# Kernel tuning notes

Hardware: AMD Instinct MI355X
Metric: run time of the kernel (lower is better)

The kernel has to match this reference:

```python
import jax, jax.numpy as jnp
import numpy as np

TEMPERATURE = 0.5
NEG_FILL = -9e15


def setup_inputs() -> dict:
    key = jax.random.key(0)
    k1, k2 = jax.random.split(key)
    B, D = 4096, 256
    z1 = jax.random.normal(k1, (B, D), dtype=jnp.float32)
    z2 = jax.random.normal(k2, (B, D), dtype=jnp.float32)
    return {"z1": z1, "z2": z2}


def reference(z1, z2):
    B = z1.shape[0]
    z = jnp.concatenate([z1, z2], axis=0)  # [2B, D]
    # cosine similarity: normalize once, then GEMM (same math as broadcast cosine_similarity,
    # torch uses eps=1e-8 clamp on norms)
    norm = jnp.maximum(jnp.linalg.norm(z, axis=1, keepdims=True), 1e-8)
    zn = z / norm
    sim = (zn @ zn.T) / TEMPERATURE  # [2B, 2B]
    # mask self-similarity on the diagonal
    idx = jnp.arange(2 * B)
    sim = sim.at[idx, idx].set(NEG_FILL)
    labels = jnp.concatenate([jnp.arange(B) + B, jnp.arange(B)], axis=0)  # [2B]
    logp = jax.nn.log_softmax(sim, axis=1)
    loss = -jnp.mean(logp[idx, labels])
    return loss
```

## Files before the change

kernel.cpp:

```cpp
#include <hip/hip_runtime.h>

#define N_TOTAL 8192
#define B_HALF  4096
#define D_DIM   256
#define BM      128
#define CSPLIT  8
#define COLS_PER_SPLIT 1024
#define NTILE   8

typedef __attribute__((ext_vector_type(4))) float f32x4;
typedef __attribute__((ext_vector_type(4))) int   int4v;
typedef __attribute__((ext_vector_type(8))) int   int8v;

#define LOG2E   1.44269504088896f
#define NLOG2E2 2.88539008177793f

#define GLOAD16(src, dst) __builtin_amdgcn_global_load_lds( \
    (const __attribute__((address_space(1))) unsigned int*)(src), \
    (__attribute__((address_space(3))) unsigned int*)(dst), 16, 0, 0)

__device__ __forceinline__ float fp8_to_f32(unsigned b) {
    unsigned s = b >> 7, e = (b >> 3) & 15, m = b & 7;
    float mag = e ? (float)(8 + m) * __int_as_float((int)((e + 117) << 23))
                  : (float)m * 0.001953125f;
    return s ? -mag : mag;
}

__global__ __launch_bounds__(256) void nrmpos_kernel(const float* __restrict__ z1,
                                                     const float* __restrict__ z2,
                                                     unsigned char* __restrict__ zn8,
                                                     float* __restrict__ pos,
                                                     float* __restrict__ self) {
    int i    = (blockIdx.x * 256 + threadIdx.x) >> 6;
    int lane = threadIdx.x & 63;
    float4 a = reinterpret_cast<const float4*>(z1 + (size_t)i * D_DIM)[lane];
    float4 b = reinterpret_cast<const float4*>(z2 + (size_t)i * D_DIM)[lane];
    float ssa = a.x * a.x + a.y * a.y + a.z * a.z + a.w * a.w;
    float ssb = b.x * b.x + b.y * b.y + b.z * b.z + b.w * b.w;
    float dab = a.x * b.x + a.y * b.y + a.z * b.z + a.w * b.w;
#pragma unroll
    for (int m = 32; m >= 1; m >>= 1) {
        ssa += __shfl_xor(ssa, m);
        ssb += __shfl_xor(ssb, m);
        dab += __shfl_xor(dab, m);
    }
    float inva = 1.0f / fmaxf(sqrtf(ssa), 1e-8f);
    float invb = 1.0f / fmaxf(sqrtf(ssb), 1e-8f);
    float sa = 1.4142135623730951f * inva;
    float sb = 1.4142135623730951f * invb;
    int pa = __builtin_amdgcn_cvt_pk_fp8_f32(a.x * sa, a.y * sa, 0, false);
    pa     = __builtin_amdgcn_cvt_pk_fp8_f32(a.z * sa, a.w * sa, pa, true);
    int pb = __builtin_amdgcn_cvt_pk_fp8_f32(b.x * sb, b.y * sb, 0, false);
    pb     = __builtin_amdgcn_cvt_pk_fp8_f32(b.z * sb, b.w * sb, pb, true);
    float sa8 = 0.0f, sb8 = 0.0f;
#pragma unroll
    for (int u = 0; u < 4; ++u) {
        float da = fp8_to_f32((unsigned)(pa >> (8 * u)) & 0xff);
        float db = fp8_to_f32((unsigned)(pb >> (8 * u)) & 0xff);
        sa8 += da * da;
        sb8 += db * db;
    }
#pragma unroll
    for (int m = 32; m >= 1; m >>= 1) {
        sa8 += __shfl_xor(sa8, m);
        sb8 += __shfl_xor(sb8, m);
    }
    *reinterpret_cast<int*>(zn8 + (size_t)i * D_DIM + lane * 4)            = pa;
    *reinterpret_cast<int*>(zn8 + (size_t)(i + B_HALF) * D_DIM + lane * 4) = pb;
    if (lane == 0) {
        float pp = 2.0f * dab * inva * invb;
        pos[i]           = pp;
        pos[i + B_HALF]  = pp;
        self[i]          = sa8;
        self[i + B_HALF] = sb8;
    }
}

__global__ __launch_bounds__(256, 2) void simexp_kernel(const unsigned char* __restrict__ zn8,
                                                        float* __restrict__ partials) {
    __shared__ __attribute__((aligned(16))) unsigned char lB[2][BM * D_DIM];
    __shared__ float red[4][64];

    const int bi = blockIdx.x;
    const int ci = blockIdx.y;
    const int tid  = threadIdx.x;
    const int lane = tid & 63;
    const int wid  = tid >> 6;
    const int wr   = wid >> 1;
    const int wc   = wid & 1;
    const int lrow16 = lane & 15;
    const int kgrp   = lane >> 4;

    const unsigned char* Abase  = zn8 + (size_t)bi * BM * D_DIM;
    const unsigned char* Bbase0 = zn8 + (size_t)ci * COLS_PER_SPLIT * D_DIM;

    int soff[8];
#pragma unroll
    for (int u = 0; u < 8; ++u) {
        const int g = tid + u * 256;
        const int r = g >> 4, c = g & 15;
        soff[u] = r * D_DIM + ((c ^ (r & 15)) << 4);
    }
    auto stageB = [&](int t, int buf) {
        const unsigned char* Bb = Bbase0 + (size_t)t * BM * D_DIM;
#pragma unroll
        for (int u = 0; u < 8; ++u)
            GLOAD16(Bb + soff[u], lB[buf] + ((tid + u * 256) << 4));
    };

    auto load32 = [&](const unsigned char* base, int row, int ck) -> int8v {
        const int c0 = ck * 8 + kgrp * 2;
        int4v lo = *reinterpret_cast<const int4v*>(
            base + row * D_DIM + (((c0 + 0) ^ lrow16) << 4));
        int4v hi = *reinterpret_cast<const int4v*>(
            base + row * D_DIM + (((c0 + 1) ^ lrow16) << 4));
        int8v r8;
        r8[0] = lo[0]; r8[1] = lo[1]; r8[2] = lo[2]; r8[3] = lo[3];
        r8[4] = hi[0]; r8[5] = hi[1]; r8[6] = hi[2]; r8[7] = hi[3];
        return r8;
    };

#pragma unroll
    for (int u = 0; u < 8; ++u)
        GLOAD16(Abase + soff[u], lB[1] + ((tid + u * 256) << 4));
    stageB(0, 0);
    __syncthreads();

    int8v aF[2][4];
#pragma unroll
    for (int ck = 0; ck < 2; ++ck)
#pragma unroll
        for (int mt = 0; mt < 4; ++mt)
            aF[ck][mt] = load32(lB[1], wr * 64 + mt * 16 + lrow16, ck);
    __syncthreads();
    stageB(1, 1);

    f32x4 acc[4][4];
    float rowacc[4][4];
#pragma unroll
    for (int mt = 0; mt < 4; ++mt)
#pragma unroll
        for (int nt = 0; nt < 4; ++nt) { acc[mt][nt] = (f32x4)(0.0f); rowacc[mt][nt] = 0.0f; }

    for (int t = 0; t < NTILE; ++t) {
        const unsigned char* Bl = lB[t & 1];

        __builtin_amdgcn_s_setprio(1);
#pragma unroll
        for (int ck = 0; ck < 2; ++ck) {
            int8v bF[4];
#pragma unroll
            for (int nt = 0; nt < 4; ++nt)
                bF[nt] = load32(Bl, wc * 64 + nt * 16 + lrow16, ck);
#pragma unroll
            for (int mt = 0; mt < 4; ++mt)
#pragma unroll
                for (int nt = 0; nt < 4; ++nt)
                    acc[mt][nt] = __builtin_amdgcn_mfma_scale_f32_16x16x128_f8f6f4(
                        aF[ck][mt], bF[nt], acc[mt][nt],
                        0, 0, 0, 127, 0, 127);
        }
        __builtin_amdgcn_s_setprio(0);

#pragma unroll
        for (int mt = 0; mt < 4; ++mt) {
#pragma unroll
            for (int r = 0; r < 4; ++r) {
                float s = 0.0f;
#pragma unroll
                for (int nt = 0; nt < 4; ++nt)
                    s += exp2f(fmaf(acc[mt][nt][r], LOG2E, -NLOG2E2));
                rowacc[mt][r] += s;
            }
#pragma unroll
            for (int nt = 0; nt < 4; ++nt) acc[mt][nt] = (f32x4)(0.0f);
        }

        if (t + 1 < NTILE) __syncthreads();
        if (t + 2 < NTILE) stageB(t + 2, t & 1);
    }

#pragma unroll
    for (int mt = 0; mt < 4; ++mt)
#pragma unroll
        for (int r = 0; r < 4; ++r) {
            float v = rowacc[mt][r];
            v += __shfl_xor(v, 1); v += __shfl_xor(v, 2);
            v += __shfl_xor(v, 4); v += __shfl_xor(v, 8);
            if (lrow16 == 0) red[wid][mt * 16 + kgrp * 4 + r] = v;
        }
    __syncthreads();
    if (tid < BM) {
        const int h = tid >> 6, l = tid & 63;
        partials[(size_t)ci * N_TOTAL + bi * BM + tid] = red[h * 2][l] + red[h * 2 + 1][l];
    }
}

__global__ __launch_bounds__(256) void lse_kernel(const float* __restrict__ partials,
                                                  const float* __restrict__ pos,
                                                  const float* __restrict__ self,
                                                  float* __restrict__ bsums) {
    int tid = threadIdx.x;
    int row = blockIdx.x * 256 + tid;
    float s = 0.0f;
#pragma unroll
    for (int c = 0; c < CSPLIT; ++c) s += partials[(size_t)c * N_TOTAL + row];
    s -= exp2f(fmaf(self[row], LOG2E, -NLOG2E2));
    float v = 2.0f + logf(s) - pos[row];
#pragma unroll
    for (int m = 32; m >= 1; m >>= 1) v += __shfl_xor(v, m);
    __shared__ float wsum[4];
    if ((tid & 63) == 0) wsum[tid >> 6] = v;
    __syncthreads();
    if (tid == 0) bsums[blockIdx.x] = wsum[0] + wsum[1] + wsum[2] + wsum[3];
}

__global__ void final_kernel(const float* __restrict__ bsums, float* __restrict__ out) {
    int tid = threadIdx.x;
    float v = (tid < N_TOTAL / 256) ? bsums[tid] : 0.0f;
#pragma unroll
    for (int m = 32; m >= 1; m >>= 1) v += __shfl_xor(v, m);
    if (tid == 0) out[0] = v * (1.0f / (float)N_TOTAL);
}

extern "C" void kernel_launch(void* const* d_in, const int* in_sizes, int n_in,
                              void* d_out, int out_size, void* d_ws, size_t ws_size,
                              hipStream_t stream) {
    const float* z1 = (const float*)d_in[0];
    const float* z2 = (const float*)d_in[1];
    float* out = (float*)d_out;

    char* ws = (char*)d_ws;
    unsigned char* zn8 = (unsigned char*)ws;
    size_t off = (size_t)N_TOTAL * D_DIM;
    float* pos = (float*)(ws + off);
    off += (size_t)N_TOTAL * sizeof(float);
    float* self = (float*)(ws + off);
    off += (size_t)N_TOTAL * sizeof(float);
    float* partials = (float*)(ws + off);
    off += (size_t)CSPLIT * N_TOTAL * sizeof(float);
    float* bsums = (float*)(ws + off);

    nrmpos_kernel<<<B_HALF / 4, 256, 0, stream>>>(z1, z2, zn8, pos, self);
    simexp_kernel<<<dim3(N_TOTAL / BM, CSPLIT), 256, 0, stream>>>(zn8, partials);
    lse_kernel<<<N_TOTAL / 256, 256, 0, stream>>>(partials, pos, self, bsums);
    final_kernel<<<1, 64, 0, stream>>>(bsums, out);
}
```

Baseline: 41.54 us.

## Exploit similarity symmetry: compute upper-triangular tiles and emit column sums too

Since the similarity matrix is symmetric, each block now computes only tiles on or above the diagonal and accumulates both row sums and column sums of exp(sim), writing the column partials into extra slots. This roughly halves the MFMA and exp work. In exchange it adds a memset of an 80-slot partials buffer, a wider reduction in lse_kernel, uneven block work (many blocks exit early), extra shared-memory reductions, and removes the setprio hints.

```diff
diff --git a/kernel.cpp b/kernel.cpp
--- a/kernel.cpp
+++ b/kernel.cpp
@@ -4,16 +4,13 @@
 #define B_HALF  4096
 #define D_DIM   256
 #define BM      128
-#define CSPLIT  8
-#define COLS_PER_SPLIT 1024
-#define NTILE   8
+#define NB      64
+#define NSLOT   80
+#define MAXT    4
 
 typedef __attribute__((ext_vector_type(4))) float f32x4;
 typedef __attribute__((ext_vector_type(4))) int   int4v;
 typedef __attribute__((ext_vector_type(8))) int   int8v;
-
-#define LOG2E   1.44269504088896f
-#define NLOG2E2 2.88539008177793f
 
 #define GLOAD16(src, dst) __builtin_amdgcn_global_load_lds( \
     (const __attribute__((address_space(1))) unsigned int*)(src), \
@@ -80,9 +77,14 @@
                                                         float* __restrict__ partials) {
     __shared__ __attribute__((aligned(16))) unsigned char lB[2][BM * D_DIM];
     __shared__ float red[4][64];
-
-    const int bi = blockIdx.x;
-    const int ci = blockIdx.y;
+    __shared__ float redc[MAXT][4][64];
+
+    const int bi  = blockIdx.x;
+    const int c   = blockIdx.y;
+    const int bj0 = bi + 4 * c;
+    if (bj0 >= NB) return;
+    const int NT  = (NB - bj0) < MAXT ? (NB - bj0) : MAXT;
+
     const int tid  = threadIdx.x;
     const int lane = tid & 63;
     const int wid  = tid >> 6;
@@ -91,18 +93,17 @@
     const int lrow16 = lane & 15;
     const int kgrp   = lane >> 4;
 
-    const unsigned char* Abase  = zn8 + (size_t)bi * BM * D_DIM;
-    const unsigned char* Bbase0 = zn8 + (size_t)ci * COLS_PER_SPLIT * D_DIM;
+    const unsigned char* Abase = zn8 + (size_t)bi * BM * D_DIM;
 
     int soff[8];
 #pragma unroll
     for (int u = 0; u < 8; ++u) {
         const int g = tid + u * 256;
-        const int r = g >> 4, c = g & 15;
-        soff[u] = r * D_DIM + ((c ^ (r & 15)) << 4);
+        const int r = g >> 4, cc = g & 15;
+        soff[u] = r * D_DIM + ((cc ^ (r & 15)) << 4);
     }
     auto stageB = [&](int t, int buf) {
-        const unsigned char* Bb = Bbase0 + (size_t)t * BM * D_DIM;
+        const unsigned char* Bb = zn8 + (size_t)(bj0 + t) * BM * D_DIM;
 #pragma unroll
         for (int u = 0; u < 8; ++u)
             GLOAD16(Bb + soff[u], lB[buf] + ((tid + u * 256) << 4));
@@ -133,7 +134,7 @@
         for (int mt = 0; mt < 4; ++mt)
             aF[ck][mt] = load32(lB[1], wr * 64 + mt * 16 + lrow16, ck);
     __syncthreads();
-    stageB(1, 1);
+    if (NT > 1) stageB(1, 1);
 
     f32x4 acc[4][4];
     float rowacc[4][4];
@@ -142,10 +143,9 @@
 #pragma unroll
         for (int nt = 0; nt < 4; ++nt) { acc[mt][nt] = (f32x4)(0.0f); rowacc[mt][nt] = 0.0f; }
 
-    for (int t = 0; t < NTILE; ++t) {
+    for (int t = 0; t < NT; ++t) {
         const unsigned char* Bl = lB[t & 1];
 
-        __builtin_amdgcn_s_setprio(1);
 #pragma unroll
         for (int ck = 0; ck < 2; ++ck) {
             int8v bF[4];
@@ -160,24 +160,36 @@
                         aF[ck][mt], bF[nt], acc[mt][nt],
                         0, 0, 0, 127, 0, 127);
         }
-        __builtin_amdgcn_s_setprio(0);
-
+
+        if (t + 1 < NT) __syncthreads();
+        if (t + 2 < NT) stageB(t + 2, t & 1);
+
+        float cs[4] = {0.0f, 0.0f, 0.0f, 0.0f};
 #pragma unroll
         for (int mt = 0; mt < 4; ++mt) {
 #pragma unroll
             for (int r = 0; r < 4; ++r) {
                 float s = 0.0f;
 #pragma unroll
-                for (int nt = 0; nt < 4; ++nt)
-                    s += exp2f(fmaf(acc[mt][nt][r], LOG2E, -NLOG2E2));
+                for (int nt = 0; nt < 4; ++nt) {
+                    float e = __expf(acc[mt][nt][r] - 2.0f);
+                    s += e;
+                    cs[nt] += e;
+                }
                 rowacc[mt][r] += s;
             }
 #pragma unroll
             for (int nt = 0; nt < 4; ++nt) acc[mt][nt] = (f32x4)(0.0f);
         }
-
-        if (t + 1 < NTILE) __syncthreads();
-        if (t + 2 < NTILE) stageB(t + 2, t & 1);
+        if (!(c == 0 && t == 0)) {
+#pragma unroll
+            for (int nt = 0; nt < 4; ++nt) {
+                float cc2 = cs[nt];
+                cc2 += __shfl_xor(cc2, 16);
+                cc2 += __shfl_xor(cc2, 32);
+                if (kgrp == 0) redc[t][wid][nt * 16 + lrow16] = cc2;
+            }
+        }
     }
 
 #pragma unroll
@@ -192,7 +204,15 @@
     __syncthreads();
     if (tid < BM) {
         const int h = tid >> 6, l = tid & 63;
-        partials[(size_t)ci * N_TOTAL + bi * BM + tid] = red[h * 2][l] + red[h * 2 + 1][l];
+        partials[(size_t)c * N_TOTAL + bi * BM + tid] = red[h * 2][l] + red[h * 2 + 1][l];
+    } else {
+        const int col = tid - BM;
+        const int wcc = col >> 6, l = col & 63;
+        for (int t = 0; t < NT; ++t) {
+            if (c == 0 && t == 0) continue;
+            partials[(size_t)(16 + bi) * N_TOTAL + (bj0 + t) * BM + col] =
+                redc[t][wcc][l] + redc[t][2 + wcc][l];
+        }
     }
 }
 
@@ -203,9 +223,9 @@
     int tid = threadIdx.x;
     int row = blockIdx.x * 256 + tid;
     float s = 0.0f;
-#pragma unroll
-    for (int c = 0; c < CSPLIT; ++c) s += partials[(size_t)c * N_TOTAL + row];
-    s -= exp2f(fmaf(self[row], LOG2E, -NLOG2E2));
+#pragma unroll 8
+    for (int c = 0; c < NSLOT; ++c) s += partials[(size_t)c * N_TOTAL + row];
+    s -= __expf(self[row] - 2.0f);
     float v = 2.0f + logf(s) - pos[row];
 #pragma unroll
     for (int m = 32; m >= 1; m >>= 1) v += __shfl_xor(v, m);
@@ -238,11 +258,12 @@
     float* self = (float*)(ws + off);
     off += (size_t)N_TOTAL * sizeof(float);
     float* partials = (float*)(ws + off);
-    off += (size_t)CSPLIT * N_TOTAL * sizeof(float);
+    off += (size_t)NSLOT * N_TOTAL * sizeof(float);
     float* bsums = (float*)(ws + off);
 
+    hipMemsetAsync(partials, 0, (size_t)NSLOT * N_TOTAL * sizeof(float), stream);
     nrmpos_kernel<<<B_HALF / 4, 256, 0, stream>>>(z1, z2, zn8, pos, self);
-    simexp_kernel<<<dim3(N_TOTAL / BM, CSPLIT), 256, 0, stream>>>(zn8, partials);
+    simexp_kernel<<<dim3(NB, 16), 256, 0, stream>>>(zn8, partials);
     lse_kernel<<<N_TOTAL / 256, 256, 0, stream>>>(partials, pos, self, bsums);
     final_kernel<<<1, 64, 0, stream>>>(bsums, out);
 }
```

Result: slower. 47.96 us (+15.5%).
